# Kernel tuning notes

Hardware: AMD Instinct MI355X
Metric: run time of the kernel (lower is better)

The kernel has to match this reference:

```python
import jax, jax.numpy as jnp
import numpy as np

EPS = 1e-8

def setup_inputs() -> dict:
    key = jax.random.key(0)
    k1, k2, k3, k4, k5 = jax.random.split(key, 5)
    B, C_in, C_out, H, W, S, K = 16, 128, 128, 128, 128, 512, 3
    return {
        "x": jax.random.normal(k1, (B, C_in, H, W), dtype=jnp.float32),
        "style": jax.random.normal(k2, (B, S), dtype=jnp.float32),
        "weight": jax.random.normal(k3, (1, C_out, C_in, K, K), dtype=jnp.float32),
        "mod_w": jax.random.normal(k4, (C_in, S), dtype=jnp.float32) * 0.05,
        "mod_b": jax.random.normal(k5, (C_in,), dtype=jnp.float32) * 0.05,
    }

def _modulated_weights(style, weight, mod_w, mod_b):
    # style: [B, S] -> s: [B, C_in]
    s = style @ mod_w.T + mod_b
    # w: [B, C_out, C_in, K, K]
    w = weight * s[:, None, :, None, None]
    # demodulation: rsqrt of sum of squares over (C_in, K, K)
    decoef = jax.lax.rsqrt(jnp.sum(w * w, axis=(2, 3, 4)) + EPS)  # [B, C_out]
    return w * decoef[:, :, None, None, None]

def _conv_one(xi, wi):
    # xi: [C_in, H, W], wi: [C_out, C_in, K, K]; 'SAME' padding (K//2)
    out = jax.lax.conv_general_dilated(
        xi[None], wi,
        window_strides=(1, 1), padding="SAME",
        dimension_numbers=("NCHW", "OIHW", "NCHW"))
    return out[0]

def reference(x, style, weight, mod_w, mod_b):
    w = _modulated_weights(style, weight, mod_w, mod_b)  # [B, C_out, C_in, K, K]
    # per-sample conv (equivalent to groups=B grouped conv in torch)
    return jax.vmap(_conv_one)(x, w)  # [B, C_out, H, W]
```

## Files before the change

kernel.cpp:

```cpp
#include <hip/hip_runtime.h>
#include <hip/hip_bf16.h>


#define Bn 16
#define Cc 128
#define HW 128
#define Sv 512

typedef __bf16 bf16x8 __attribute__((ext_vector_type(8)));
typedef float f32x4 __attribute__((ext_vector_type(4)));
typedef float f4 __attribute__((ext_vector_type(4)));
typedef int int4v __attribute__((ext_vector_type(4)));

static __device__ __forceinline__ unsigned short bf16bits(float f) {
    return __builtin_bit_cast(unsigned short, __float2bfloat16(f));
}

__global__ __launch_bounds__(128) void k_style(const float* __restrict__ style,
                                               const float* __restrict__ mod_w,
                                               const float* __restrict__ mod_b,
                                               float* __restrict__ s_out) {
    int b = blockIdx.x;
    int ci = threadIdx.x;
    __shared__ float st[Sv];
    for (int k = threadIdx.x; k < Sv; k += 128)
        st[k] = style[b * Sv + k];
    __syncthreads();
    float acc = mod_b[ci];
    const float* mw = mod_w + (size_t)ci * Sv;
    for (int k = 0; k < Sv; k++)
        acc += st[k] * mw[k];
    s_out[b * Cc + ci] = acc;
}

__global__ __launch_bounds__(128) void k_mod(const float* __restrict__ weight,
                                             const float* __restrict__ s,
                                             __hip_bfloat16* __restrict__ wsW) {
    int b = blockIdx.x >> 7;
    int co = blockIdx.x & 127;
    int ci = threadIdx.x;
    float sv = s[b * Cc + ci];
    const float* wp = weight + ((size_t)co * Cc + ci) * 9;
    float wv[9];
    float ss = 0.f;
#pragma unroll
    for (int j = 0; j < 9; j++) {
        wv[j] = wp[j] * sv;
        ss += wv[j] * wv[j];
    }
    __shared__ float red[128];
    red[ci] = ss;
    __syncthreads();
    for (int s2 = 64; s2 > 0; s2 >>= 1) {
        if (ci < s2) red[ci] += red[ci + s2];
        __syncthreads();
    }
    float dec = rsqrtf(red[0] + 1e-8f);
#pragma unroll
    for (int j = 0; j < 9; j++) {
        wsW[(((size_t)b * 9 + j) * Cc + co) * Cc + ci] = __float2bfloat16(wv[j] * dec);
    }
}

__global__ __launch_bounds__(256, 2) void k_conv(const float* __restrict__ x,
                                                 const __hip_bfloat16* __restrict__ wsW,
                                                 float* __restrict__ out) {
    const int LDW = 136;
    __shared__ __align__(16) __bf16 Xs[128 * 128];
    __shared__ __align__(16) __bf16 Ws[128 * LDW];

    int bx = blockIdx.x;
    int b = bx >> 7, h = bx & 127;
    int t = threadIdx.x;
    int lane = t & 63;
    int wvid = t >> 6;
    int wave_m = wvid >> 1, wave_n = wvid & 1;
    int l15 = lane & 15, quad = lane >> 4;

    f32x4 acc[4][4] = {};
    const bf16x8 zfrag = {};

    const float* xb = x + (size_t)b * (Cc * HW * HW);
    const __hip_bfloat16* wbase = wsW + (size_t)b * 9 * (Cc * Cc);

    for (int kh = 0; kh < 3; kh++) {
        int hp = h + kh - 1;
        if ((unsigned)hp >= (unsigned)HW) continue;

        __syncthreads();
        const float* xr = xb + (size_t)hp * HW;
#pragma unroll
        for (int it = 0; it < 8; it++) {
            int id = it * 256 + t;
            int cp = id >> 5;
            int seg = id & 31;
            int ci0 = cp * 2;
            const float* p0 = xr + (size_t)ci0 * (HW * HW) + seg * 4;
            f4 v0 = *(const f4*)p0;
            f4 v1 = *(const f4*)(p0 + HW * HW);
            int cg = cp >> 2;
            int sub = (cp & 3) * 2;
#pragma unroll
            for (int j = 0; j < 4; j++) {
                int w = seg * 4 + j;
                int sw = (w ^ (w >> 3)) & 7;
                int off = w * 128 + ((cg ^ sw) << 3) + sub;
                unsigned int pv = (unsigned int)bf16bits(v0[j]) | ((unsigned int)bf16bits(v1[j]) << 16);
                *(unsigned int*)(&Xs[off]) = pv;
            }
        }

        for (int kw = 0; kw < 3; kw++) {
            __syncthreads();
            const __hip_bfloat16* wsrc = wbase + (size_t)(kh * 3 + kw) * (Cc * Cc);
#pragma unroll
            for (int it = 0; it < 8; it++) {
                int id = it * 256 + t;
                int wr = id >> 4, seg = id & 15;
                int4v v = *(const int4v*)(wsrc + id * 8);
                *(int4v*)(&Ws[wr * LDW + seg * 8]) = v;
            }
            __syncthreads();
#pragma unroll
            for (int ks = 0; ks < 4; ks++) {
                int k0 = ks * 32 + quad * 8;
                int kg = k0 >> 3;
                bf16x8 a[4], bfr[4];
#pragma unroll
                for (int mi = 0; mi < 4; mi++) {
                    int co = wave_m * 64 + mi * 16 + l15;
                    a[mi] = *(const bf16x8*)(&Ws[co * LDW + k0]);
                }
#pragma unroll
                for (int ni = 0; ni < 4; ni++) {
                    int w = wave_n * 64 + ni * 16 + l15;
                    int wp = w + kw - 1;
                    bool ok = (unsigned)wp < (unsigned)HW;
                    int wc = ok ? wp : 0;
                    int sw = (wc ^ (wc >> 3)) & 7;
                    bf16x8 bv = *(const bf16x8*)(&Xs[wc * 128 + ((kg ^ sw) << 3)]);
                    bfr[ni] = ok ? bv : zfrag;
                }
#pragma unroll
                for (int mi = 0; mi < 4; mi++)
#pragma unroll
                    for (int ni = 0; ni < 4; ni++)
                        acc[mi][ni] = __builtin_amdgcn_mfma_f32_16x16x32_bf16(a[mi], bfr[ni], acc[mi][ni], 0, 0, 0);
            }
        }
    }

    float* ob = out + (size_t)b * (Cc * HW * HW) + h * HW;
#pragma unroll
    for (int mi = 0; mi < 4; mi++) {
#pragma unroll
        for (int ni = 0; ni < 4; ni++) {
            int w = wave_n * 64 + ni * 16 + l15;
#pragma unroll
            for (int r = 0; r < 4; r++) {
                int co = wave_m * 64 + mi * 16 + quad * 4 + r;
                ob[(size_t)co * (HW * HW) + w] = acc[mi][ni][r];
            }
        }
    }
}

extern "C" void kernel_launch(void* const* d_in, const int* in_sizes, int n_in,
                              void* d_out, int out_size, void* d_ws, size_t ws_size,
                              hipStream_t stream) {
    const float* x      = (const float*)d_in[0];
    const float* style  = (const float*)d_in[1];
    const float* weight = (const float*)d_in[2];
    const float* mod_w  = (const float*)d_in[3];
    const float* mod_b  = (const float*)d_in[4];
    float* out = (float*)d_out;

    float* s_ws = (float*)d_ws;
    __hip_bfloat16* wsW = (__hip_bfloat16*)((char*)d_ws + 8192);

    k_style<<<Bn, 128, 0, stream>>>(style, mod_w, mod_b, s_ws);
    k_mod<<<Bn * Cc, 128, 0, stream>>>(weight, s_ws, wsW);
    k_conv<<<Bn * HW, 256, 0, stream>>>(x, wsW, out);
}
```

Measured before the change: 323.4 us.

## Stage weights via global_load_lds with pre-swizzled layout and pad X rows

```diff
diff --git a/kernel.cpp b/kernel.cpp
--- a/kernel.cpp
+++ b/kernel.cpp
@@ -9,28 +9,34 @@
 
 typedef __bf16 bf16x8 __attribute__((ext_vector_type(8)));
 typedef float f32x4 __attribute__((ext_vector_type(4)));
-typedef float f4 __attribute__((ext_vector_type(4)));
-typedef int int4v __attribute__((ext_vector_type(4)));
+typedef unsigned short ushort8 __attribute__((ext_vector_type(8)));
 
 static __device__ __forceinline__ unsigned short bf16bits(float f) {
     return __builtin_bit_cast(unsigned short, __float2bfloat16(f));
 }
 
-__global__ __launch_bounds__(128) void k_style(const float* __restrict__ style,
-                                               const float* __restrict__ mod_w,
-                                               const float* __restrict__ mod_b,
-                                               float* __restrict__ s_out) {
-    int b = blockIdx.x;
-    int ci = threadIdx.x;
-    __shared__ float st[Sv];
-    for (int k = threadIdx.x; k < Sv; k += 128)
-        st[k] = style[b * Sv + k];
-    __syncthreads();
-    float acc = mod_b[ci];
+static __device__ __forceinline__ void gl_lds16(const void* g, void* l) {
+    __builtin_amdgcn_global_load_lds(
+        (const __attribute__((address_space(1))) unsigned int*)g,
+        (__attribute__((address_space(3))) unsigned int*)l, 16, 0, 0);
+}
+
+__global__ __launch_bounds__(64) void k_style(const float* __restrict__ style,
+                                              const float* __restrict__ mod_w,
+                                              const float* __restrict__ mod_b,
+                                              float* __restrict__ s_out) {
+    int b = blockIdx.x >> 7, ci = blockIdx.x & 127;
+    int lane = threadIdx.x;
+    const float* st = style + (size_t)b * Sv;
     const float* mw = mod_w + (size_t)ci * Sv;
-    for (int k = 0; k < Sv; k++)
-        acc += st[k] * mw[k];
-    s_out[b * Cc + ci] = acc;
+    float acc = 0.f;
+#pragma unroll
+    for (int k = 0; k < Sv; k += 64)
+        acc += st[k + lane] * mw[k + lane];
+#pragma unroll
+    for (int off = 32; off > 0; off >>= 1)
+        acc += __shfl_down(acc, off, 64);
+    if (lane == 0) s_out[b * Cc + ci] = acc + mod_b[ci];
 }
 
 __global__ __launch_bounds__(128) void k_mod(const float* __restrict__ weight,
@@ -56,18 +62,18 @@
         __syncthreads();
     }
     float dec = rsqrtf(red[0] + 1e-8f);
+    int pos = ((((ci >> 3) ^ (co & 7)) << 3) | (ci & 7));
 #pragma unroll
     for (int j = 0; j < 9; j++) {
-        wsW[(((size_t)b * 9 + j) * Cc + co) * Cc + ci] = __float2bfloat16(wv[j] * dec);
+        wsW[(((size_t)b * 9 + j) * Cc + co) * Cc + pos] = __float2bfloat16(wv[j] * dec);
     }
 }
 
 __global__ __launch_bounds__(256, 2) void k_conv(const float* __restrict__ x,
                                                  const __hip_bfloat16* __restrict__ wsW,
                                                  float* __restrict__ out) {
-    const int LDW = 136;
-    __shared__ __align__(16) __bf16 Xs[128 * 128];
-    __shared__ __align__(16) __bf16 Ws[128 * LDW];
+    __shared__ __align__(16) __bf16 Xs[130 * 128];
+    __shared__ __align__(16) __bf16 Ws[128 * 128];
 
     int bx = blockIdx.x;
     int b = bx >> 7, h = bx & 127;
@@ -78,10 +84,15 @@
     int l15 = lane & 15, quad = lane >> 4;
 
     f32x4 acc[4][4] = {};
-    const bf16x8 zfrag = {};
 
     const float* xb = x + (size_t)b * (Cc * HW * HW);
     const __hip_bfloat16* wbase = wsW + (size_t)b * 9 * (Cc * Cc);
+
+    if (t < 32) {
+        int row = (t < 16) ? 0 : 129;
+        int g = t & 15;
+        *(bf16x8*)(&Xs[row * 128 + g * 8]) = (bf16x8){};
+    }
 
     for (int kh = 0; kh < 3; kh++) {
         int hp = h + kh - 1;
@@ -92,22 +103,16 @@
 #pragma unroll
         for (int it = 0; it < 8; it++) {
             int id = it * 256 + t;
-            int cp = id >> 5;
-            int seg = id & 31;
-            int ci0 = cp * 2;
-            const float* p0 = xr + (size_t)ci0 * (HW * HW) + seg * 4;
-            f4 v0 = *(const f4*)p0;
-            f4 v1 = *(const f4*)(p0 + HW * HW);
-            int cg = cp >> 2;
-            int sub = (cp & 3) * 2;
+            int w = id & 127;
+            int cig = id >> 7;
+            const float* p = xr + (size_t)cig * 8 * (HW * HW) + w;
+            ushort8 pk;
 #pragma unroll
-            for (int j = 0; j < 4; j++) {
-                int w = seg * 4 + j;
-                int sw = (w ^ (w >> 3)) & 7;
-                int off = w * 128 + ((cg ^ sw) << 3) + sub;
-                unsigned int pv = (unsigned int)bf16bits(v0[j]) | ((unsigned int)bf16bits(v1[j]) << 16);
-                *(unsigned int*)(&Xs[off]) = pv;
-            }
+            for (int j = 0; j < 8; j++)
+                pk[j] = bf16bits(p[(size_t)j * (HW * HW)]);
+            int row = w + 1;
+            int g2 = cig ^ (row & 7);
+            *(bf16x8*)(&Xs[row * 128 + (g2 << 3)]) = __builtin_bit_cast(bf16x8, pk);
         }
 
         for (int kw = 0; kw < 3; kw++) {
@@ -115,31 +120,23 @@
             const __hip_bfloat16* wsrc = wbase + (size_t)(kh * 3 + kw) * (Cc * Cc);
 #pragma unroll
             for (int it = 0; it < 8; it++) {
-                int id = it * 256 + t;
-                int wr = id >> 4, seg = id & 15;
-                int4v v = *(const int4v*)(wsrc + id * 8);
-                *(int4v*)(&Ws[wr * LDW + seg * 8]) = v;
+                int chunk = wvid * 8 + it;
+                gl_lds16(wsrc + chunk * 512 + lane * 8, &Ws[chunk * 512]);
             }
             __syncthreads();
 #pragma unroll
             for (int ks = 0; ks < 4; ks++) {
-                int k0 = ks * 32 + quad * 8;
-                int kg = k0 >> 3;
+                int kg = ks * 4 + quad;
                 bf16x8 a[4], bfr[4];
 #pragma unroll
                 for (int mi = 0; mi < 4; mi++) {
                     int co = wave_m * 64 + mi * 16 + l15;
-                    a[mi] = *(const bf16x8*)(&Ws[co * LDW + k0]);
+                    a[mi] = *(const bf16x8*)(&Ws[co * 128 + ((kg ^ (co & 7)) << 3)]);
                 }
 #pragma unroll
                 for (int ni = 0; ni < 4; ni++) {
-                    int w = wave_n * 64 + ni * 16 + l15;
-                    int wp = w + kw - 1;
-                    bool ok = (unsigned)wp < (unsigned)HW;
-                    int wc = ok ? wp : 0;
-                    int sw = (wc ^ (wc >> 3)) & 7;
-                    bf16x8 bv = *(const bf16x8*)(&Xs[wc * 128 + ((kg ^ sw) << 3)]);
-                    bfr[ni] = ok ? bv : zfrag;
+                    int row = wave_n * 64 + ni * 16 + l15 + kw;
+                    bfr[ni] = *(const bf16x8*)(&Xs[row * 128 + ((kg ^ (row & 7)) << 3)]);
                 }
 #pragma unroll
                 for (int mi = 0; mi < 4; mi++)
@@ -178,7 +175,7 @@
     float* s_ws = (float*)d_ws;
     __hip_bfloat16* wsW = (__hip_bfloat16*)((char*)d_ws + 8192);
 
-    k_style<<<Bn, 128, 0, stream>>>(style, mod_w, mod_b, s_ws);
+    k_style<<<Bn * Cc, 64, 0, stream>>>(style, mod_w, mod_b, s_ws);
     k_mod<<<Bn * Cc, 128, 0, stream>>>(weight, s_ws, wsW);
     k_conv<<<Bn * HW, 256, 0, stream>>>(x, wsW, out);
 }
```

Measured after the change: 298.3 us. 7.8% less time.
